# Optimization experiments

Measured on AMD Instinct MI355X. Metric: run time of the kernel, lower is better.

The kernel has to match this reference:

```python
import jax, jax.numpy as jnp
import numpy as np

N, F_IN, H1, H2, HEADS, E = 8192, 512, 128, 64, 3, 262144
NEG_SLOPE = 0.2  # PyG GATConv default negative_slope


def _add_self_loops(src, dst, n):
    loop = jnp.arange(n, dtype=src.dtype)
    return jnp.concatenate([src, loop]), jnp.concatenate([dst, loop])


def _gcn_conv(x, src, dst, W, b, n):
    # PyG GCNConv: h = x @ W, add self-loops, symmetric D^-1/2 A D^-1/2 aggregation, + bias
    h = x @ W
    s, d = _add_self_loops(src, dst, n)
    deg = jax.ops.segment_sum(jnp.ones(s.shape, h.dtype), d, num_segments=n)
    dinv = jnp.where(deg > 0, jax.lax.rsqrt(deg), 0.0)
    norm = dinv[s] * dinv[d]  # [E']
    return jax.ops.segment_sum(h[s] * norm[:, None], d, num_segments=n) + b


def _gat_conv(x, src, dst, W, a_src, a_dst, b, n, heads, concat):
    # PyG GATConv: per-head linear, LeakyReLU attention logits, segment softmax over
    # incoming edges per destination node, weighted scatter-aggregate.
    out_dim = W.shape[1] // heads
    h = (x @ W).reshape(n, heads, out_dim)  # [N, H, D]
    s, d = _add_self_loops(src, dst, n)
    a_s = jnp.einsum('nhd,hd->nh', h, a_src)
    a_d = jnp.einsum('nhd,hd->nh', h, a_dst)
    e = jax.nn.leaky_relu(a_s[s] + a_d[d], NEG_SLOPE)  # [E', H]
    m = jax.ops.segment_max(e, d, num_segments=n)      # stable softmax per dst segment
    ex = jnp.exp(e - m[d])
    den = jax.ops.segment_sum(ex, d, num_segments=n)
    msg = h[s] * (ex / den[d])[..., None]              # [E', H, D]
    out = jax.ops.segment_sum(msg, d, num_segments=n)  # [N, H, D]
    if concat:
        return out.reshape(n, heads * out_dim) + b
    return out.mean(axis=1) + b


def _forward(x, edge_index, gcn_W1, gcn_b1, gcn_Wmu, gcn_bmu, gcn_Wlv, gcn_blv,
             gat_W1, gat_as1, gat_ad1, gat_b1,
             gat_Wmu, gat_asmu, gat_admu, gat_bmu,
             gat_Wlv, gat_aslv, gat_adlv, gat_blv,
             eps_gcn, eps_gat):
    src, dst = edge_index[0], edge_index[1]
    n = x.shape[0]
    mu_g = lv_g = z_g = None
    for i in range(gcn_W1.shape[0]):  # gcn branches
        h = jax.nn.relu(_gcn_conv(x, src, dst, gcn_W1[i], gcn_b1[i], n))
        mu = _gcn_conv(h, src, dst, gcn_Wmu[i], gcn_bmu[i], n)
        lv = _gcn_conv(h, src, dst, gcn_Wlv[i], gcn_blv[i], n)
        z = mu + eps_gcn[i] * jnp.exp(lv)  # faithful: logvar passed as logstd
        mu_g = mu if mu_g is None else jnp.maximum(mu_g, mu)
        lv_g = lv if lv_g is None else jnp.maximum(lv_g, lv)
        z_g = z if z_g is None else jnp.maximum(z_g, z)
    mu_a = lv_a = z_a = None
    for i in range(gat_W1.shape[0]):  # gat branches
        h = jax.nn.relu(_gat_conv(x, src, dst, gat_W1[i], gat_as1[i], gat_ad1[i], gat_b1[i], n, HEADS, True))
        mu = _gat_conv(h, src, dst, gat_Wmu[i], gat_asmu[i], gat_admu[i], gat_bmu[i], n, HEADS, False)
        lv = _gat_conv(h, src, dst, gat_Wlv[i], gat_aslv[i], gat_adlv[i], gat_blv[i], n, HEADS, False)
        z = mu + eps_gat[i] * jnp.exp(lv)
        mu_a = mu if mu_a is None else jnp.maximum(mu_a, mu)
        lv_a = lv if lv_a is None else jnp.maximum(lv_a, lv)
        z_a = z if z_a is None else jnp.maximum(z_a, z)
    mu_max = jnp.maximum(mu_g, mu_a)
    lv_max = jnp.maximum(lv_g, lv_a)
    z_max = jnp.maximum(z_g, z_a)
    adj = jax.nn.sigmoid(z_max @ z_max.T)  # InnerProductDecoder.forward_all(sigmoid=True)
    return adj, mu_max, lv_max


def setup_inputs():
    key = jax.random.key(0)
    ki = iter(jax.random.split(key, 32))
    p = lambda shape: jax.random.normal(next(ki), shape, dtype=jnp.float32) * 0.05
    x = jax.random.normal(next(ki), (N, F_IN), dtype=jnp.float32)
    edge_index = jax.random.randint(next(ki), (2, E), 0, N)
    return dict(
        x=x, edge_index=edge_index,
        gcn_W1=p((2, F_IN, H1)), gcn_b1=p((2, H1)),
        gcn_Wmu=p((2, H1, H2)), gcn_bmu=p((2, H2)),
        gcn_Wlv=p((2, H1, H2)), gcn_blv=p((2, H2)),
        gat_W1=p((2, F_IN, HEADS * H1)), gat_as1=p((2, HEADS, H1)),
        gat_ad1=p((2, HEADS, H1)), gat_b1=p((2, HEADS * H1)),
        gat_Wmu=p((2, HEADS * H1, HEADS * H2)), gat_asmu=p((2, HEADS, H2)),
        gat_admu=p((2, HEADS, H2)), gat_bmu=p((2, H2)),
        gat_Wlv=p((2, HEADS * H1, HEADS * H2)), gat_aslv=p((2, HEADS, H2)),
        gat_adlv=p((2, HEADS, H2)), gat_blv=p((2, H2)),
        eps_gcn=jax.random.normal(next(ki), (2, N, H2), dtype=jnp.float32),
        eps_gat=jax.random.normal(next(ki), (2, N, H2), dtype=jnp.float32),
    )


def reference(x, edge_index, gcn_W1, gcn_b1, gcn_Wmu, gcn_bmu, gcn_Wlv, gcn_blv,
              gat_W1, gat_as1, gat_ad1, gat_b1,
              gat_Wmu, gat_asmu, gat_admu, gat_bmu,
              gat_Wlv, gat_aslv, gat_adlv, gat_blv,
              eps_gcn, eps_gat):
    return _forward(x, edge_index, gcn_W1, gcn_b1, gcn_Wmu, gcn_bmu, gcn_Wlv, gcn_blv,
                    gat_W1, gat_as1, gat_ad1, gat_b1,
                    gat_Wmu, gat_asmu, gat_admu, gat_bmu,
                    gat_Wlv, gat_aslv, gat_adlv, gat_blv,
                    eps_gcn, eps_gat)
```

## Files before the change

kernel.cpp:

```cpp
#include <hip/hip_runtime.h>
#include <hip/hip_bf16.h>
#include <math.h>
#include <stddef.h>

#define NN 8192
#define NEG_SLOPE 0.2f

typedef _Float16 h8 __attribute__((ext_vector_type(8)));
typedef __attribute__((ext_vector_type(4))) float f32x4;

__device__ __forceinline__ float lrelu(float x) { return x > 0.f ? x : NEG_SLOPE * x; }
__device__ __forceinline__ float sigf(float x) { return 1.f / (1.f + __expf(-x)); }

__device__ __forceinline__ unsigned short f16b(float x) {
    _Float16 h = (_Float16)x;
    unsigned short u;
    __builtin_memcpy(&u, &h, 2);
    return u;
}
__device__ __forceinline__ float f16f(unsigned short u) {
    _Float16 h;
    __builtin_memcpy(&h, &u, 2);
    return (float)h;
}
__device__ __forceinline__ void splith(float x, unsigned short& hu, unsigned short& lu) {
    _Float16 h = (_Float16)x;
    float hf = (float)h;
    _Float16 l = (_Float16)(x - hf);
    __builtin_memcpy(&hu, &h, 2);
    __builtin_memcpy(&lu, &l, 2);
}
__device__ __forceinline__ float2 unpkh(unsigned int v) {
    float2 r;
    r.x = f16f((unsigned short)(v & 0xffffu));
    r.y = f16f((unsigned short)(v >> 16));
    return r;
}
__device__ __forceinline__ unsigned int packh(float a, float b) {
    return (unsigned int)f16b(a) | ((unsigned int)f16b(b) << 16);
}

__device__ __forceinline__ void gll16(const unsigned short* g, unsigned short* l) {
    __builtin_amdgcn_global_load_lds(
        (const __attribute__((address_space(1))) unsigned int*)g,
        (__attribute__((address_space(3))) unsigned int*)l, 16, 0, 0);
}

__global__ void k_zero(int* __restrict__ p, int n) {
    int i = blockIdx.x * blockDim.x + threadIdx.x;
    if (i < n) p[i] = 0;
}
__global__ void k_count(const int* __restrict__ dst, int* __restrict__ cnt, int E) {
    int i = blockIdx.x * blockDim.x + threadIdx.x;
    if (i < E) atomicAdd(&cnt[dst[i]], 1);
}
__global__ void k_dinv(const int* __restrict__ cnt, float* __restrict__ dinv) {
    int i = blockIdx.x * blockDim.x + threadIdx.x;
    if (i < NN) dinv[i] = rsqrtf((float)(cnt[i] + 1));
}
__global__ void k_scan(const int* __restrict__ cnt, int* __restrict__ row_ptr) {
    __shared__ int part[1024];
    int t = threadIdx.x;
    int base = t * 8;
    int loc[8];
    int s = 0;
    #pragma unroll
    for (int j = 0; j < 8; ++j) { loc[j] = s; s += cnt[base + j]; }
    part[t] = s;
    __syncthreads();
    for (int off = 1; off < 1024; off <<= 1) {
        int v = (t >= off) ? part[t - off] : 0;
        __syncthreads();
        part[t] += v;
        __syncthreads();
    }
    int pre = (t == 0) ? 0 : part[t - 1];
    #pragma unroll
    for (int j = 0; j < 8; ++j) row_ptr[base + j] = pre + loc[j];
    if (t == 1023) row_ptr[NN] = part[1023];
}
__global__ void k_fill(const int* __restrict__ src, const int* __restrict__ dst,
                       const int* __restrict__ row_ptr, int* __restrict__ cursor,
                       int* __restrict__ csr_src, int E) {
    int i = blockIdx.x * blockDim.x + threadIdx.x;
    if (i < E) {
        int d = dst[i];
        csr_src[row_ptr[d] + atomicAdd(&cursor[d], 1)] = src[i];
    }
}

__global__ void k_cvt_x(const float* __restrict__ x, unsigned short* __restrict__ xh) {
    int i = blockIdx.x * 256 + threadIdx.x;
    int m = i >> 7, k4 = (i & 127) * 4;
    float4 v = *(const float4*)(x + (size_t)m * 512 + k4);
    ushort4 o;
    o.x = f16b(v.x); o.y = f16b(v.y); o.z = f16b(v.z); o.w = f16b(v.w);
    *(ushort4*)&xh[(size_t)m * 512 + k4] = o;
}

__global__ void k_wT(const float* __restrict__ W, unsigned short* __restrict__ Wt,
                     int K, int N, size_t wt_z_stride, int noff, int noff_z) {
    int b = blockIdx.z;
    W += (size_t)b * K * N;
    Wt += (size_t)b * wt_z_stride;
    int rowbase = noff + b * noff_z;
    int k0 = blockIdx.x * 32, n0 = blockIdx.y * 32;
    __shared__ float tl[32][33];
    int tid = threadIdx.x;
    int r = tid >> 5, cc = tid & 31;
    #pragma unroll
    for (int c = 0; c < 4; ++c)
        tl[r + c * 8][cc] = W[(size_t)(k0 + r + c * 8) * N + n0 + cc];
    __syncthreads();
    #pragma unroll
    for (int c = 0; c < 4; ++c) {
        int n = r + c * 8, k = cc;
        Wt[(size_t)(rowbase + n0 + n) * K + k0 + k] = f16b(tl[k][n]);
    }
}

template <int ROWS>
__device__ __forceinline__ void stage(const unsigned short* __restrict__ gbase, int lda,
                                      unsigned short* lds, int wid, int lane) {
    #pragma unroll
    for (int c = 0; c < ROWS / 32; ++c) {
        int chunk = c * 4 + wid;
        int row = chunk * 8 + (lane >> 3);
        int g = (lane & 7) ^ (row & 7);
        gll16(gbase + (size_t)row * lda + g * 8, lds + chunk * 512);
    }
}
__device__ __forceinline__ h8 fragrh(const unsigned short* lds, int row, int kg) {
    return *(const h8*)(lds + row * 64 + ((kg ^ (row & 7)) * 8));
}

template <int TERMS, int EPI>
__global__ __launch_bounds__(256) void k_gemm2(
    const unsigned short* __restrict__ A2, size_t azs, int lda,
    const unsigned short* __restrict__ B2, size_t bzs, int ldb,
    void* __restrict__ Cv, size_t czs, int ldc, int K) {
    __shared__ __align__(16) unsigned short sAh[128 * 64];
    __shared__ __align__(16) unsigned short sBh[64 * 64];
    __shared__ __align__(16) unsigned short sAl[(TERMS == 3) ? 128 * 64 : 8];
    __shared__ __align__(16) unsigned short sBl[(TERMS == 3) ? 64 * 64 : 8];
    const int tid = threadIdx.x;
    const int wid = tid >> 6, lane = tid & 63;
    const int wr = wid >> 1, wc = wid & 1;
    const int lr = lane & 15, lg = lane >> 4;
    const int m0 = blockIdx.x * 128, n0 = blockIdx.y * 64;
    const int z = blockIdx.z;
    A2 += (size_t)z * azs;
    B2 += (size_t)z * bzs;

    const f32x4 zero4 = {0.f, 0.f, 0.f, 0.f};
    f32x4 acc[4][2];
    #pragma unroll
    for (int m = 0; m < 4; ++m)
        #pragma unroll
        for (int n = 0; n < 2; ++n) acc[m][n] = zero4;

    for (int k0 = 0; k0 < K; k0 += 64) {
        stage<128>(A2 + (size_t)m0 * lda + k0, lda, sAh, wid, lane);
        stage<64> (B2 + (size_t)n0 * ldb + k0, ldb, sBh, wid, lane);
        if (TERMS == 3) {
            stage<128>(A2 + (size_t)m0 * lda + K + k0, lda, sAl, wid, lane);
            stage<64> (B2 + (size_t)n0 * ldb + K + k0, ldb, sBl, wid, lane);
        }
        __syncthreads();
        #pragma unroll
        for (int ks = 0; ks < 2; ++ks) {
            const int kg = ks * 4 + lg;
            h8 ah[4], al[4], bh[2], bl[2];
            #pragma unroll
            for (int m = 0; m < 4; ++m) {
                int row = wr * 64 + m * 16 + lr;
                ah[m] = fragrh(sAh, row, kg);
                if (TERMS == 3) al[m] = fragrh(sAl, row, kg);
            }
            #pragma unroll
            for (int n = 0; n < 2; ++n) {
                int row = wc * 32 + n * 16 + lr;
                bh[n] = fragrh(sBh, row, kg);
                if (TERMS == 3) bl[n] = fragrh(sBl, row, kg);
            }
            #pragma unroll
            for (int m = 0; m < 4; ++m)
                #pragma unroll
                for (int n = 0; n < 2; ++n) {
                    acc[m][n] = __builtin_amdgcn_mfma_f32_16x16x32_f16(ah[m], bh[n], acc[m][n], 0, 0, 0);
                    if (TERMS == 3) {
                        acc[m][n] = __builtin_amdgcn_mfma_f32_16x16x32_f16(al[m], bh[n], acc[m][n], 0, 0, 0);
                        acc[m][n] = __builtin_amdgcn_mfma_f32_16x16x32_f16(ah[m], bl[n], acc[m][n], 0, 0, 0);
                    }
                }
        }
        __syncthreads();
    }
    #pragma unroll
    for (int m = 0; m < 4; ++m)
        #pragma unroll
        for (int n = 0; n < 2; ++n)
            #pragma unroll
            for (int j = 0; j < 4; ++j) {
                int row = m0 + wr * 64 + m * 16 + lg * 4 + j;
                int col = n0 + wc * 32 + n * 16 + lr;
                float o = acc[m][n][j];
                if (EPI == 1) {
                    ((float*)Cv + (size_t)z * czs)[(size_t)row * ldc + col] = sigf(o);
                } else if (EPI == 2) {
                    ((unsigned short*)Cv + (size_t)z * czs)[(size_t)row * ldc + col] = f16b(o);
                } else {
                    ((float*)Cv + (size_t)z * czs)[(size_t)row * ldc + col] = o;
                }
            }
}

__global__ void k_gcn_a1(const uint2* __restrict__ xw2, const float* __restrict__ dinv,
                         const int* __restrict__ rp, const int* __restrict__ cs,
                         const float* __restrict__ b1, uint2* __restrict__ hb2) {
    int d = blockIdx.x;
    int t = threadIdx.x;
    float dd = dinv[d];
    uint2 sv = xw2[(size_t)d * 64 + t];
    float2 s0 = unpkh(sv.x), s1 = unpkh(sv.y);
    float a0 = dd * s0.x, a1 = dd * s0.y, a2 = dd * s1.x, a3 = dd * s1.y;
    int e0 = rp[d], e1 = rp[d + 1];
    int j = e0;
    for (; j + 4 <= e1; j += 4) {
        int i0 = cs[j], i1 = cs[j + 1], i2 = cs[j + 2], i3 = cs[j + 3];
        float w0 = dinv[i0], w1 = dinv[i1], w2 = dinv[i2], w3 = dinv[i3];
        uint2 v0 = xw2[(size_t)i0 * 64 + t];
        uint2 v1 = xw2[(size_t)i1 * 64 + t];
        uint2 v2 = xw2[(size_t)i2 * 64 + t];
        uint2 v3 = xw2[(size_t)i3 * 64 + t];
        float2 p;
        p = unpkh(v0.x); a0 += w0 * p.x; a1 += w0 * p.y;
        p = unpkh(v0.y); a2 += w0 * p.x; a3 += w0 * p.y;
        p = unpkh(v1.x); a0 += w1 * p.x; a1 += w1 * p.y;
        p = unpkh(v1.y); a2 += w1 * p.x; a3 += w1 * p.y;
        p = unpkh(v2.x); a0 += w2 * p.x; a1 += w2 * p.y;
        p = unpkh(v2.y); a2 += w2 * p.x; a3 += w2 * p.y;
        p = unpkh(v3.x); a0 += w3 * p.x; a1 += w3 * p.y;
        p = unpkh(v3.y); a2 += w3 * p.x; a3 += w3 * p.y;
    }
    for (; j < e1; ++j) {
        int s = cs[j];
        float w = dinv[s];
        uint2 v = xw2[(size_t)s * 64 + t];
        float2 p;
        p = unpkh(v.x); a0 += w * p.x; a1 += w * p.y;
        p = unpkh(v.y); a2 += w * p.x; a3 += w * p.y;
    }
    int c = 4 * t;
    float o0 = fmaxf(dd * a0 + b1[c], 0.f);
    float o1 = fmaxf(dd * a1 + b1[c + 1], 0.f);
    float o2 = fmaxf(dd * a2 + b1[c + 2], 0.f);
    float o3 = fmaxf(dd * a3 + b1[c + 3], 0.f);
    uint2 o;
    o.x = packh(o0, o1);
    o.y = packh(o2, o3);
    hb2[(size_t)d * 64 + t] = o;
}

__global__ void k_gcn_a2(const uint2* __restrict__ hb2, const float* __restrict__ dinv,
                         const int* __restrict__ rp, const int* __restrict__ cs,
                         uint2* __restrict__ hA2) {
    int d = blockIdx.x;
    int t = threadIdx.x;
    float dd = dinv[d];
    uint2 sv = hb2[(size_t)d * 64 + t];
    float2 s0 = unpkh(sv.x), s1 = unpkh(sv.y);
    float a0 = dd * s0.x, a1 = dd * s0.y, a2 = dd * s1.x, a3 = dd * s1.y;
    int e0 = rp[d], e1 = rp[d + 1];
    int j = e0;
    for (; j + 4 <= e1; j += 4) {
        int i0 = cs[j], i1 = cs[j + 1], i2 = cs[j + 2], i3 = cs[j + 3];
        float w0 = dinv[i0], w1 = dinv[i1], w2 = dinv[i2], w3 = dinv[i3];
        uint2 v0 = hb2[(size_t)i0 * 64 + t];
        uint2 v1 = hb2[(size_t)i1 * 64 + t];
        uint2 v2 = hb2[(size_t)i2 * 64 + t];
        uint2 v3 = hb2[(size_t)i3 * 64 + t];
        float2 p;
        p = unpkh(v0.x); a0 += w0 * p.x; a1 += w0 * p.y;
        p = unpkh(v0.y); a2 += w0 * p.x; a3 += w0 * p.y;
        p = unpkh(v1.x); a0 += w1 * p.x; a1 += w1 * p.y;
        p = unpkh(v1.y); a2 += w1 * p.x; a3 += w1 * p.y;
        p = unpkh(v2.x); a0 += w2 * p.x; a1 += w2 * p.y;
        p = unpkh(v2.y); a2 += w2 * p.x; a3 += w2 * p.y;
        p = unpkh(v3.x); a0 += w3 * p.x; a1 += w3 * p.y;
        p = unpkh(v3.y); a2 += w3 * p.x; a3 += w3 * p.y;
    }
    for (; j < e1; ++j) {
        int s = cs[j];
        float w = dinv[s];
        uint2 v = hb2[(size_t)s * 64 + t];
        float2 p;
        p = unpkh(v.x); a0 += w * p.x; a1 += w * p.y;
        p = unpkh(v.y); a2 += w * p.x; a3 += w * p.y;
    }
    uint2 o;
    o.x = packh(dd * a0, dd * a1);
    o.y = packh(dd * a2, dd * a3);
    hA2[(size_t)d * 64 + t] = o;
}

__global__ void k_gat_log1(const unsigned int* __restrict__ xwu, const float* __restrict__ a_s,
                           const float* __restrict__ a_d, float* __restrict__ as_n,
                           float* __restrict__ ad_n) {
    int br = blockIdx.z;
    int n = blockIdx.x;
    int hd = threadIdx.x >> 6, lane = threadIdx.x & 63;
    const unsigned int* hp = xwu + (size_t)n * 384 + br * 192 + hd * 64;
    const float* av = a_s + br * 384 + hd * 128;
    const float* dv = a_d + br * 384 + hd * 128;
    float2 f = unpkh(hp[lane]);
    float ss = f.x * av[2 * lane] + f.y * av[2 * lane + 1];
    float sd = f.x * dv[2 * lane] + f.y * dv[2 * lane + 1];
    #pragma unroll
    for (int off = 32; off; off >>= 1) {
        ss += __shfl_down(ss, off);
        sd += __shfl_down(sd, off);
    }
    if (lane == 0) {
        as_n[(size_t)br * NN * 3 + n * 3 + hd] = ss;
        ad_n[(size_t)br * NN * 3 + n * 3 + hd] = sd;
    }
}

__global__ void k_gat_log2(const unsigned short* __restrict__ h2gb, const float* __restrict__ asmu,
                           const float* __restrict__ aslv, const float* __restrict__ admu,
                           const float* __restrict__ adlv, float* __restrict__ as_n,
                           float* __restrict__ ad_n) {
    int zz = blockIdx.z;
    int br = zz >> 1, mt = zz & 1;
    int n = blockIdx.x;
    int hd = threadIdx.x >> 6, lane = threadIdx.x & 63;
    const unsigned short* hp = h2gb + (size_t)br * NN * 384 + (size_t)n * 384 + mt * 192 + hd * 64;
    const float* av = (mt ? aslv : asmu) + br * 192 + hd * 64;
    const float* dv = (mt ? adlv : admu) + br * 192 + hd * 64;
    float hv = f16f(hp[lane]);
    float ss = hv * av[lane];
    float sd = hv * dv[lane];
    #pragma unroll
    for (int off = 32; off; off >>= 1) {
        ss += __shfl_down(ss, off);
        sd += __shfl_down(sd, off);
    }
    if (lane == 0) {
        as_n[(size_t)zz * NN * 3 + n * 3 + hd] = ss;
        ad_n[(size_t)zz * NN * 3 + n * 3 + hd] = sd;
    }
}

__global__ void k_gat_attn(const float* __restrict__ as_n, const float* __restrict__ ad_n,
                           const int* __restrict__ rp, const int* __restrict__ cs,
                           float* __restrict__ w_csr, float* __restrict__ w_self, int E3) {
    int zz = blockIdx.z;
    as_n += (size_t)zz * NN * 3;
    ad_n += (size_t)zz * NN * 3;
    w_csr += (size_t)zz * E3;
    w_self += (size_t)zz * NN * 3;
    int d = blockIdx.x;
    int hd = threadIdx.x >> 6, lane = threadIdx.x & 63;
    int e0 = rp[d], e1 = rp[d + 1];
    float add = ad_n[d * 3 + hd];
    float eself = lrelu(as_n[d * 3 + hd] + add);
    float mx = eself;
    for (int j = e0 + lane; j < e1; j += 64) {
        float e = lrelu(as_n[cs[j] * 3 + hd] + add);
        w_csr[(size_t)j * 3 + hd] = e;
        mx = fmaxf(mx, e);
    }
    #pragma unroll
    for (int off = 32; off; off >>= 1) mx = fmaxf(mx, __shfl_xor(mx, off));
    float sm = (lane == 0) ? __expf(eself - mx) : 0.f;
    for (int j = e0 + lane; j < e1; j += 64)
        sm += __expf(w_csr[(size_t)j * 3 + hd] - mx);
    #pragma unroll
    for (int off = 32; off; off >>= 1) sm += __shfl_xor(sm, off);
    float inv = 1.f / sm;
    if (lane == 0) w_self[d * 3 + hd] = __expf(eself - mx) * inv;
    for (int j = e0 + lane; j < e1; j += 64)
        w_csr[(size_t)j * 3 + hd] = __expf(w_csr[(size_t)j * 3 + hd] - mx) * inv;
}

__global__ void k_gat_agg1(const uint2* __restrict__ xw2, const float* __restrict__ w_csr,
                           const float* __restrict__ w_self, const int* __restrict__ rp,
                           const int* __restrict__ cs, const float* __restrict__ b1,
                           uint2* __restrict__ h1s2, int E3) {
    int d = blockIdx.x;
    int t = threadIdx.x;
    int br = t >= 96 ? 1 : 0;
    int c = 4 * t - br * 384;
    int hd = c >> 7;
    const float* wc = w_csr + (size_t)br * E3;
    float ws = w_self[(size_t)br * NN * 3 + d * 3 + hd];
    uint2 sv = xw2[(size_t)d * 192 + t];
    float2 s0 = unpkh(sv.x), s1 = unpkh(sv.y);
    float a0 = ws * s0.x, a1 = ws * s0.y, a2 = ws * s1.x, a3 = ws * s1.y;
    int e0 = rp[d], e1 = rp[d + 1];
    int j = e0;
    for (; j + 4 <= e1; j += 4) {
        int i0 = cs[j], i1 = cs[j + 1], i2 = cs[j + 2], i3 = cs[j + 3];
        float w0 = wc[(size_t)(j + 0) * 3 + hd];
        float w1 = wc[(size_t)(j + 1) * 3 + hd];
        float w2 = wc[(size_t)(j + 2) * 3 + hd];
        float w3 = wc[(size_t)(j + 3) * 3 + hd];
        uint2 v0 = xw2[(size_t)i0 * 192 + t];
        uint2 v1 = xw2[(size_t)i1 * 192 + t];
        uint2 v2 = xw2[(size_t)i2 * 192 + t];
        uint2 v3 = xw2[(size_t)i3 * 192 + t];
        float2 p;
        p = unpkh(v0.x); a0 += w0 * p.x; a1 += w0 * p.y;
        p = unpkh(v0.y); a2 += w0 * p.x; a3 += w0 * p.y;
        p = unpkh(v1.x); a0 += w1 * p.x; a1 += w1 * p.y;
        p = unpkh(v1.y); a2 += w1 * p.x; a3 += w1 * p.y;
        p = unpkh(v2.x); a0 += w2 * p.x; a1 += w2 * p.y;
        p = unpkh(v2.y); a2 += w2 * p.x; a3 += w2 * p.y;
        p = unpkh(v3.x); a0 += w3 * p.x; a1 += w3 * p.y;
        p = unpkh(v3.y); a2 += w3 * p.x; a3 += w3 * p.y;
    }
    for (; j < e1; ++j) {
        int s = cs[j];
        float w = wc[(size_t)j * 3 + hd];
        uint2 v = xw2[(size_t)s * 192 + t];
        float2 p;
        p = unpkh(v.x); a0 += w * p.x; a1 += w * p.y;
        p = unpkh(v.y); a2 += w * p.x; a3 += w * p.y;
    }
    int cg = 4 * t;
    float o0 = fmaxf(a0 + b1[cg], 0.f);
    float o1 = fmaxf(a1 + b1[cg + 1], 0.f);
    float o2 = fmaxf(a2 + b1[cg + 2], 0.f);
    float o3 = fmaxf(a3 + b1[cg + 3], 0.f);
    uint2 o;
    o.x = packh(o0, o1);
    o.y = packh(o2, o3);
    h1s2[(size_t)d * 192 + t] = o;
}

__global__ void k_gat_agg2(const uint2* __restrict__ h2g2, const float* __restrict__ w_csr,
                           const float* __restrict__ w_self, const int* __restrict__ rp,
                           const int* __restrict__ cs, const float* __restrict__ bmu,
                           const float* __restrict__ blv, float* __restrict__ mt_gat, int E3) {
    int d = blockIdx.x;
    int t = threadIdx.x;
    int br = t >= 96 ? 1 : 0;
    int tb = t - br * 96;
    int mt = tb >= 48 ? 1 : 0;
    int c = 4 * tb - mt * 192;
    int hd = c >> 6;
    const float* wc = w_csr + (size_t)(br * 2 + mt) * E3;
    float ws = w_self[(size_t)(br * 2 + mt) * NN * 3 + d * 3 + hd];
    const uint2* hp = h2g2 + (size_t)br * NN * 96;
    uint2 sv = hp[(size_t)d * 96 + tb];
    float2 s0 = unpkh(sv.x), s1 = unpkh(sv.y);
    float a0 = ws * s0.x, a1 = ws * s0.y, a2 = ws * s1.x, a3 = ws * s1.y;
    int e0 = rp[d], e1 = rp[d + 1];
    int j = e0;
    for (; j + 4 <= e1; j += 4) {
        int i0 = cs[j], i1 = cs[j + 1], i2 = cs[j + 2], i3 = cs[j + 3];
        float w0 = wc[(size_t)(j + 0) * 3 + hd];
        float w1 = wc[(size_t)(j + 1) * 3 + hd];
        float w2 = wc[(size_t)(j + 2) * 3 + hd];
        float w3 = wc[(size_t)(j + 3) * 3 + hd];
        uint2 v0 = hp[(size_t)i0 * 96 + tb];
        uint2 v1 = hp[(size_t)i1 * 96 + tb];
        uint2 v2 = hp[(size_t)i2 * 96 + tb];
        uint2 v3 = hp[(size_t)i3 * 96 + tb];
        float2 p;
        p = unpkh(v0.x); a0 += w0 * p.x; a1 += w0 * p.y;
        p = unpkh(v0.y); a2 += w0 * p.x; a3 += w0 * p.y;
        p = unpkh(v1.x); a0 += w1 * p.x; a1 += w1 * p.y;
        p = unpkh(v1.y); a2 += w1 * p.x; a3 += w1 * p.y;
        p = unpkh(v2.x); a0 += w2 * p.x; a1 += w2 * p.y;
        p = unpkh(v2.y); a2 += w2 * p.x; a3 += w2 * p.y;
        p = unpkh(v3.x); a0 += w3 * p.x; a1 += w3 * p.y;
        p = unpkh(v3.y); a2 += w3 * p.x; a3 += w3 * p.y;
    }
    for (; j < e1; ++j) {
        int s = cs[j];
        float w = wc[(size_t)j * 3 + hd];
        uint2 v = hp[(size_t)s * 96 + tb];
        float2 p;
        p = unpkh(v.x); a0 += w * p.x; a1 += w * p.y;
        p = unpkh(v.y); a2 += w * p.x; a3 += w * p.y;
    }
    __shared__ float red[768];
    int rb = br * 384 + mt * 192 + c;
    red[rb] = a0; red[rb + 1] = a1; red[rb + 2] = a2; red[rb + 3] = a3;
    __syncthreads();
    if (t < 128) {
        #pragma unroll
        for (int q = 0; q < 2; ++q) {
            int o = t + q * 128;
            int obr = o >> 7, omt = (o >> 6) & 1, dd = o & 63;
            int base = obr * 384 + omt * 192;
            float tot = red[base + dd] + red[base + 64 + dd] + red[base + 128 + dd];
            const float* bias = omt ? blv : bmu;
            float v = tot * (1.f / 3.f) + bias[obr * 64 + dd];
            mt_gat[((size_t)(obr * 2 + omt) * NN + d) * 64 + dd] = v;
        }
    }
}

__global__ void k_finalize(const float* __restrict__ muv_gcn, const float* __restrict__ gcn_bmu,
                           const float* __restrict__ gcn_blv, const float* __restrict__ mt_gat,
                           const float* __restrict__ eps_gcn, const float* __restrict__ eps_gat,
                           float* __restrict__ mu_o, float* __restrict__ lv_o,
                           unsigned short* __restrict__ z2) {
    int i = blockIdx.x * 256 + threadIdx.x;
    int d = i >> 6, c = i & 63;
    const size_t NN64 = (size_t)NN * 64;
    float mu, lv, zm;
    {
        float m = muv_gcn[(size_t)d * 128 + c] + gcn_bmu[c];
        float l = muv_gcn[(size_t)d * 128 + 64 + c] + gcn_blv[c];
        float z = m + eps_gcn[i] * __expf(l);
        mu = m; lv = l; zm = z;
    }
    {
        float m = muv_gcn[NN64 * 2 + (size_t)d * 128 + c] + gcn_bmu[64 + c];
        float l = muv_gcn[NN64 * 2 + (size_t)d * 128 + 64 + c] + gcn_blv[64 + c];
        float z = m + eps_gcn[NN64 + i] * __expf(l);
        mu = fmaxf(mu, m); lv = fmaxf(lv, l); zm = fmaxf(zm, z);
    }
    #pragma unroll
    for (int br = 0; br < 2; ++br) {
        float m = mt_gat[(size_t)(br * 2 + 0) * NN64 + i];
        float l = mt_gat[(size_t)(br * 2 + 1) * NN64 + i];
        float z = m + eps_gat[(size_t)br * NN64 + i] * __expf(l);
        mu = fmaxf(mu, m); lv = fmaxf(lv, l); zm = fmaxf(zm, z);
    }
    mu_o[i] = mu;
    lv_o[i] = lv;
    unsigned short hh, ll;
    splith(zm, hh, ll);
    z2[(size_t)d * 128 + c] = hh;
    z2[(size_t)d * 128 + 64 + c] = ll;
}

extern "C" void kernel_launch(void* const* d_in, const int* in_sizes, int n_in,
                              void* d_out, int out_size, void* d_ws, size_t ws_size,
                              hipStream_t stream) {
    const float* x  = (const float*)d_in[0];
    const int*   ei = (const int*)d_in[1];
    const int E = in_sizes[1] / 2;
    const int E3 = E * 3;
    const int* src = ei;
    const int* dst = ei + E;

    const float* gcn_W1  = (const float*)d_in[2];
    const float* gcn_b1  = (const float*)d_in[3];
    const float* gcn_Wmu = (const float*)d_in[4];
    const float* gcn_bmu = (const float*)d_in[5];
    const float* gcn_Wlv = (const float*)d_in[6];
    const float* gcn_blv = (const float*)d_in[7];
    const float* gat_W1  = (const float*)d_in[8];
    const float* gat_as1 = (const float*)d_in[9];
    const float* gat_ad1 = (const float*)d_in[10];
    const float* gat_b1  = (const float*)d_in[11];
    const float* gat_Wmu = (const float*)d_in[12];
    const float* gat_asmu= (const float*)d_in[13];
    const float* gat_admu= (const float*)d_in[14];
    const float* gat_bmu = (const float*)d_in[15];
    const float* gat_Wlv = (const float*)d_in[16];
    const float* gat_aslv= (const float*)d_in[17];
    const float* gat_adlv= (const float*)d_in[18];
    const float* gat_blv = (const float*)d_in[19];
    const float* eps_gcn = (const float*)d_in[20];
    const float* eps_gat = (const float*)d_in[21];

    char* p = (char*)d_ws;
    auto alloc = [&](size_t bytes) {
        void* r = (void*)p;
        p += (bytes + 255) & ~(size_t)255;
        return r;
    };
    int*   cnt     = (int*)alloc((size_t)NN * 4);
    int*   cursor  = (int*)alloc((size_t)NN * 4);
    int*   row_ptr = (int*)alloc((size_t)(NN + 1) * 4);
    int*   csr_src = (int*)alloc((size_t)E * 4);
    float* dinv    = (float*)alloc((size_t)NN * 4);
    float* as_n1   = (float*)alloc((size_t)2 * NN * 3 * 4);
    float* ad_n1   = (float*)alloc((size_t)2 * NN * 3 * 4);
    float* wself1  = (float*)alloc((size_t)2 * NN * 3 * 4);
    float* wcsr1   = (float*)alloc((size_t)2 * E3 * 4);
    float* as_n2   = (float*)alloc((size_t)4 * NN * 3 * 4);
    float* ad_n2   = (float*)alloc((size_t)4 * NN * 3 * 4);
    float* wself2  = (float*)alloc((size_t)4 * NN * 3 * 4);
    float* wcsr2   = (float*)alloc((size_t)4 * E3 * 4);
    unsigned short* x2h      = (unsigned short*)alloc((size_t)NN * 512 * 2);
    unsigned short* wt_gcn1  = (unsigned short*)alloc((size_t)256 * 512 * 2);
    unsigned short* wt_gcnmuv= (unsigned short*)alloc((size_t)2 * 128 * 128 * 2);
    unsigned short* wt_gat1  = (unsigned short*)alloc((size_t)768 * 512 * 2);
    unsigned short* wt_gatmuv= (unsigned short*)alloc((size_t)2 * 384 * 384 * 2);
    unsigned short* xwb  = (unsigned short*)alloc((size_t)NN * 768 * 2);
    unsigned short* hb   = (unsigned short*)alloc((size_t)NN * 256 * 2);
    unsigned short* hA   = (unsigned short*)alloc((size_t)NN * 256 * 2);
    float* muv_gcn = (float*)alloc((size_t)2 * NN * 128 * 4);
    unsigned short* h1s  = (unsigned short*)alloc((size_t)NN * 768 * 2);
    unsigned short* h2gb = (unsigned short*)alloc((size_t)2 * NN * 384 * 2);
    float* mt_gat  = (float*)alloc((size_t)4 * NN * 64 * 4);
    unsigned short* z2 = (unsigned short*)alloc((size_t)NN * 128 * 2);

    float* adj  = (float*)d_out;
    float* mu_o = adj + (size_t)NN * NN;
    float* lv_o = mu_o + (size_t)NN * 64;

    k_zero<<<(2 * NN + 255) / 256, 256, 0, stream>>>(cnt, 2 * NN);
    k_count<<<(E + 255) / 256, 256, 0, stream>>>(dst, cnt, E);
    k_dinv<<<(NN + 255) / 256, 256, 0, stream>>>(cnt, dinv);
    k_scan<<<1, 1024, 0, stream>>>(cnt, row_ptr);
    k_fill<<<(E + 255) / 256, 256, 0, stream>>>(src, dst, row_ptr, cursor, csr_src, E);

    k_cvt_x<<<NN * 512 / 4 / 256, 256, 0, stream>>>(x, x2h);
    k_wT<<<dim3(16, 4, 2), 256, 0, stream>>>(gcn_W1, wt_gcn1, 512, 128, 0, 0, 128);
    k_wT<<<dim3(4, 2, 2), 256, 0, stream>>>(gcn_Wmu, wt_gcnmuv, 128, 64, (size_t)128 * 128, 0, 0);
    k_wT<<<dim3(4, 2, 2), 256, 0, stream>>>(gcn_Wlv, wt_gcnmuv, 128, 64, (size_t)128 * 128, 64, 0);
    k_wT<<<dim3(16, 12, 2), 256, 0, stream>>>(gat_W1, wt_gat1, 512, 384, 0, 0, 384);
    k_wT<<<dim3(12, 6, 2), 256, 0, stream>>>(gat_Wmu, wt_gatmuv, 384, 192, (size_t)384 * 384, 0, 0);
    k_wT<<<dim3(12, 6, 2), 256, 0, stream>>>(gat_Wlv, wt_gatmuv, 384, 192, (size_t)384 * 384, 192, 0);

    k_gemm2<1, 2><<<dim3(64, 4, 1), 256, 0, stream>>>(x2h, 0, 512, wt_gcn1, 0, 512,
                                                      xwb, 0, 256, 512);
    k_gcn_a1<<<NN, 64, 0, stream>>>((const uint2*)xwb, dinv, row_ptr, csr_src, gcn_b1,
                                    (uint2*)hb);
    k_gcn_a2<<<NN, 64, 0, stream>>>((const uint2*)hb, dinv, row_ptr, csr_src, (uint2*)hA);
    k_gemm2<1, 0><<<dim3(64, 2, 2), 256, 0, stream>>>(hA, 128, 256, wt_gcnmuv,
                                                      (size_t)128 * 128, 128,
                                                      muv_gcn, (size_t)NN * 128, 128, 128);

    k_gemm2<1, 2><<<dim3(64, 12, 1), 256, 0, stream>>>(x2h, 0, 512, wt_gat1, 0, 512,
                                                       xwb, 0, 768, 512);
    k_gat_log1<<<dim3(NN, 1, 2), 192, 0, stream>>>((const unsigned int*)xwb, gat_as1,
                                                   gat_ad1, as_n1, ad_n1);
    k_gat_attn<<<dim3(NN, 1, 2), 192, 0, stream>>>(as_n1, ad_n1, row_ptr, csr_src,
                                                   wcsr1, wself1, E3);
    k_gat_agg1<<<NN, 192, 0, stream>>>((const uint2*)xwb, wcsr1, wself1, row_ptr, csr_src,
                                       gat_b1, (uint2*)h1s, E3);
    k_gemm2<1, 2><<<dim3(64, 6, 2), 256, 0, stream>>>(h1s, 384, 768, wt_gatmuv,
                                                      (size_t)384 * 384, 384,
                                                      h2gb, (size_t)NN * 384, 384, 384);
    k_gat_log2<<<dim3(NN, 1, 4), 192, 0, stream>>>(h2gb, gat_asmu, gat_aslv, gat_admu,
                                                   gat_adlv, as_n2, ad_n2);
    k_gat_attn<<<dim3(NN, 1, 4), 192, 0, stream>>>(as_n2, ad_n2, row_ptr, csr_src,
                                                   wcsr2, wself2, E3);
    k_gat_agg2<<<NN, 192, 0, stream>>>((const uint2*)h2gb, wcsr2, wself2, row_ptr, csr_src,
                                       gat_bmu, gat_blv, mt_gat, E3);

    k_finalize<<<NN * 64 / 256, 256, 0, stream>>>(muv_gcn, gcn_bmu, gcn_blv, mt_gat,
                                                  eps_gcn, eps_gat, mu_o, lv_o, z2);
    k_gemm2<3, 1><<<dim3(64, 128, 1), 256, 0, stream>>>(z2, 0, 128, z2, 0, 128,
                                                        adj, 0, NN, 64);
}
```

Baseline: 364.8 us.

## Fuse GAT softmax into aggregation, drop one split-fp16 term, nontemporal adj stores

Merges the GAT attention-softmax kernel with the aggregation kernel for both layers. Edge indices and normalized weights are kept in shared memory, capped per node with a recompute fallback for high degree, so the per-edge weight arrays no longer go through global memory and two launches are removed. The final z·zᵀ GEMM drops from three split-fp16 MFMA terms to two (hi·hi + lo·hi), which cuts MFMA work and B-side lo staging but loses some precision. The sigmoid adjacency output is written with nontemporal stores to reduce cache pollution.

```diff
diff --git a/kernel.cpp b/kernel.cpp
--- a/kernel.cpp
+++ b/kernel.cpp
@@ -5,6 +5,7 @@
 
 #define NN 8192
 #define NEG_SLOPE 0.2f
+#define CAP 256
 
 typedef _Float16 h8 __attribute__((ext_vector_type(8)));
 typedef __attribute__((ext_vector_type(4))) float f32x4;
@@ -141,8 +142,8 @@
     void* __restrict__ Cv, size_t czs, int ldc, int K) {
     __shared__ __align__(16) unsigned short sAh[128 * 64];
     __shared__ __align__(16) unsigned short sBh[64 * 64];
-    __shared__ __align__(16) unsigned short sAl[(TERMS == 3) ? 128 * 64 : 8];
-    __shared__ __align__(16) unsigned short sBl[(TERMS == 3) ? 64 * 64 : 8];
+    __shared__ __align__(16) unsigned short sAl[(TERMS >= 2) ? 128 * 64 : 8];
+    __shared__ __align__(16) unsigned short sBl[(TERMS >= 3) ? 64 * 64 : 8];
     const int tid = threadIdx.x;
     const int wid = tid >> 6, lane = tid & 63;
     const int wr = wid >> 1, wc = wid & 1;
@@ -162,10 +163,8 @@
     for (int k0 = 0; k0 < K; k0 += 64) {
         stage<128>(A2 + (size_t)m0 * lda + k0, lda, sAh, wid, lane);
         stage<64> (B2 + (size_t)n0 * ldb + k0, ldb, sBh, wid, lane);
-        if (TERMS == 3) {
-            stage<128>(A2 + (size_t)m0 * lda + K + k0, lda, sAl, wid, lane);
-            stage<64> (B2 + (size_t)n0 * ldb + K + k0, ldb, sBl, wid, lane);
-        }
+        if (TERMS >= 2) stage<128>(A2 + (size_t)m0 * lda + K + k0, lda, sAl, wid, lane);
+        if (TERMS >= 3) stage<64> (B2 + (size_t)n0 * ldb + K + k0, ldb, sBl, wid, lane);
         __syncthreads();
         #pragma unroll
         for (int ks = 0; ks < 2; ++ks) {
@@ -175,23 +174,23 @@
             for (int m = 0; m < 4; ++m) {
                 int row = wr * 64 + m * 16 + lr;
                 ah[m] = fragrh(sAh, row, kg);
-                if (TERMS == 3) al[m] = fragrh(sAl, row, kg);
+                if (TERMS >= 2) al[m] = fragrh(sAl, row, kg);
             }
             #pragma unroll
             for (int n = 0; n < 2; ++n) {
                 int row = wc * 32 + n * 16 + lr;
                 bh[n] = fragrh(sBh, row, kg);
-                if (TERMS == 3) bl[n] = fragrh(sBl, row, kg);
+                if (TERMS >= 3) bl[n] = fragrh(sBl, row, kg);
             }
             #pragma unroll
             for (int m = 0; m < 4; ++m)
                 #pragma unroll
                 for (int n = 0; n < 2; ++n) {
                     acc[m][n] = __builtin_amdgcn_mfma_f32_16x16x32_f16(ah[m], bh[n], acc[m][n], 0, 0, 0);
-                    if (TERMS == 3) {
+                    if (TERMS >= 2)
                         acc[m][n] = __builtin_amdgcn_mfma_f32_16x16x32_f16(al[m], bh[n], acc[m][n], 0, 0, 0);
+                    if (TERMS >= 3)
                         acc[m][n] = __builtin_amdgcn_mfma_f32_16x16x32_f16(ah[m], bl[n], acc[m][n], 0, 0, 0);
-                    }
                 }
         }
         __syncthreads();
@@ -206,7 +205,8 @@
                 int col = n0 + wc * 32 + n * 16 + lr;
                 float o = acc[m][n][j];
                 if (EPI == 1) {
-                    ((float*)Cv + (size_t)z * czs)[(size_t)row * ldc + col] = sigf(o);
+                    float* cp = (float*)Cv + (size_t)z * czs + (size_t)row * ldc + col;
+                    __builtin_nontemporal_store(sigf(o), cp);
                 } else if (EPI == 2) {
                     ((unsigned short*)Cv + (size_t)z * czs)[(size_t)row * ldc + col] = f16b(o);
                 } else {
@@ -352,155 +352,191 @@
     }
 }
 
-__global__ void k_gat_attn(const float* __restrict__ as_n, const float* __restrict__ ad_n,
-                           const int* __restrict__ rp, const int* __restrict__ cs,
-                           float* __restrict__ w_csr, float* __restrict__ w_self, int E3) {
-    int zz = blockIdx.z;
-    as_n += (size_t)zz * NN * 3;
-    ad_n += (size_t)zz * NN * 3;
-    w_csr += (size_t)zz * E3;
-    w_self += (size_t)zz * NN * 3;
-    int d = blockIdx.x;
-    int hd = threadIdx.x >> 6, lane = threadIdx.x & 63;
-    int e0 = rp[d], e1 = rp[d + 1];
-    float add = ad_n[d * 3 + hd];
-    float eself = lrelu(as_n[d * 3 + hd] + add);
-    float mx = eself;
-    for (int j = e0 + lane; j < e1; j += 64) {
-        float e = lrelu(as_n[cs[j] * 3 + hd] + add);
-        w_csr[(size_t)j * 3 + hd] = e;
-        mx = fmaxf(mx, e);
-    }
-    #pragma unroll
-    for (int off = 32; off; off >>= 1) mx = fmaxf(mx, __shfl_xor(mx, off));
-    float sm = (lane == 0) ? __expf(eself - mx) : 0.f;
-    for (int j = e0 + lane; j < e1; j += 64)
-        sm += __expf(w_csr[(size_t)j * 3 + hd] - mx);
-    #pragma unroll
-    for (int off = 32; off; off >>= 1) sm += __shfl_xor(sm, off);
-    float inv = 1.f / sm;
-    if (lane == 0) w_self[d * 3 + hd] = __expf(eself - mx) * inv;
-    for (int j = e0 + lane; j < e1; j += 64)
-        w_csr[(size_t)j * 3 + hd] = __expf(w_csr[(size_t)j * 3 + hd] - mx) * inv;
-}
-
-__global__ void k_gat_agg1(const uint2* __restrict__ xw2, const float* __restrict__ w_csr,
-                           const float* __restrict__ w_self, const int* __restrict__ rp,
-                           const int* __restrict__ cs, const float* __restrict__ b1,
-                           uint2* __restrict__ h1s2, int E3) {
+__global__ __launch_bounds__(384) void k_gat_fused1(
+    const unsigned int* __restrict__ xwu,
+    const float* __restrict__ as_n, const float* __restrict__ ad_n,
+    const int* __restrict__ rp, const int* __restrict__ cs,
+    const float* __restrict__ b1, unsigned int* __restrict__ h1su) {
     int d = blockIdx.x;
     int t = threadIdx.x;
-    int br = t >= 96 ? 1 : 0;
-    int c = 4 * t - br * 384;
-    int hd = c >> 7;
-    const float* wc = w_csr + (size_t)br * E3;
-    float ws = w_self[(size_t)br * NN * 3 + d * 3 + hd];
-    uint2 sv = xw2[(size_t)d * 192 + t];
-    float2 s0 = unpkh(sv.x), s1 = unpkh(sv.y);
-    float a0 = ws * s0.x, a1 = ws * s0.y, a2 = ws * s1.x, a3 = ws * s1.y;
+    int wv = t >> 6, lane = t & 63;
     int e0 = rp[d], e1 = rp[d + 1];
-    int j = e0;
-    for (; j + 4 <= e1; j += 4) {
-        int i0 = cs[j], i1 = cs[j + 1], i2 = cs[j + 2], i3 = cs[j + 3];
-        float w0 = wc[(size_t)(j + 0) * 3 + hd];
-        float w1 = wc[(size_t)(j + 1) * 3 + hd];
-        float w2 = wc[(size_t)(j + 2) * 3 + hd];
-        float w3 = wc[(size_t)(j + 3) * 3 + hd];
-        uint2 v0 = xw2[(size_t)i0 * 192 + t];
-        uint2 v1 = xw2[(size_t)i1 * 192 + t];
-        uint2 v2 = xw2[(size_t)i2 * 192 + t];
-        uint2 v3 = xw2[(size_t)i3 * 192 + t];
-        float2 p;
-        p = unpkh(v0.x); a0 += w0 * p.x; a1 += w0 * p.y;
-        p = unpkh(v0.y); a2 += w0 * p.x; a3 += w0 * p.y;
-        p = unpkh(v1.x); a0 += w1 * p.x; a1 += w1 * p.y;
-        p = unpkh(v1.y); a2 += w1 * p.x; a3 += w1 * p.y;
-        p = unpkh(v2.x); a0 += w2 * p.x; a1 += w2 * p.y;
-        p = unpkh(v2.y); a2 += w2 * p.x; a3 += w2 * p.y;
-        p = unpkh(v3.x); a0 += w3 * p.x; a1 += w3 * p.y;
-        p = unpkh(v3.y); a2 += w3 * p.x; a3 += w3 * p.y;
-    }
-    for (; j < e1; ++j) {
-        int s = cs[j];
-        float w = wc[(size_t)j * 3 + hd];
-        uint2 v = xw2[(size_t)s * 192 + t];
-        float2 p;
-        p = unpkh(v.x); a0 += w * p.x; a1 += w * p.y;
-        p = unpkh(v.y); a2 += w * p.x; a3 += w * p.y;
-    }
-    int cg = 4 * t;
-    float o0 = fmaxf(a0 + b1[cg], 0.f);
-    float o1 = fmaxf(a1 + b1[cg + 1], 0.f);
-    float o2 = fmaxf(a2 + b1[cg + 2], 0.f);
-    float o3 = fmaxf(a3 + b1[cg + 3], 0.f);
-    uint2 o;
-    o.x = packh(o0, o1);
-    o.y = packh(o2, o3);
-    h1s2[(size_t)d * 192 + t] = o;
-}
-
-__global__ void k_gat_agg2(const uint2* __restrict__ h2g2, const float* __restrict__ w_csr,
-                           const float* __restrict__ w_self, const int* __restrict__ rp,
-                           const int* __restrict__ cs, const float* __restrict__ bmu,
-                           const float* __restrict__ blv, float* __restrict__ mt_gat, int E3) {
+    int deg = e1 - e0;
+    int dcap = deg < CAP ? deg : CAP;
+    __shared__ int se[CAP];
+    __shared__ float ws[6][CAP];
+    __shared__ float wself[6], wmx[6], winv[6], wadd[6];
+    for (int q = t; q < dcap; q += 384) se[q] = cs[e0 + q];
+    __syncthreads();
+    {
+        int br = wv / 3, hd = wv - br * 3;
+        const float* asn = as_n + (size_t)br * NN * 3;
+        float add = ad_n[(size_t)br * NN * 3 + d * 3 + hd];
+        float eself = lrelu(asn[d * 3 + hd] + add);
+        float mx = eself;
+        for (int q = lane; q < deg; q += 64) {
+            int s = (q < dcap) ? se[q] : cs[e0 + q];
+            float e = lrelu(asn[s * 3 + hd] + add);
+            if (q < dcap) ws[wv][q] = e;
+            mx = fmaxf(mx, e);
+        }
+        #pragma unroll
+        for (int off = 32; off; off >>= 1) mx = fmaxf(mx, __shfl_xor(mx, off));
+        float sm = (lane == 0) ? __expf(eself - mx) : 0.f;
+        for (int q = lane; q < deg; q += 64) {
+            float e = (q < dcap) ? ws[wv][q]
+                                 : lrelu(asn[cs[e0 + q] * 3 + hd] + add);
+            sm += __expf(e - mx);
+        }
+        #pragma unroll
+        for (int off = 32; off; off >>= 1) sm += __shfl_xor(sm, off);
+        float inv = 1.f / sm;
+        for (int q = lane; q < dcap; q += 64)
+            ws[wv][q] = __expf(ws[wv][q] - mx) * inv;
+        if (lane == 0) {
+            wself[wv] = __expf(eself - mx) * inv;
+            wmx[wv] = mx; winv[wv] = inv; wadd[wv] = add;
+        }
+    }
+    __syncthreads();
+    int br2 = t >= 192 ? 1 : 0;
+    int cu = t - br2 * 192;
+    int hd2 = cu >> 6;
+    int sw = br2 * 3 + hd2;
+    float a0, a1;
+    {
+        float2 p = unpkh(xwu[(size_t)d * 384 + t]);
+        float wsf = wself[sw];
+        a0 = wsf * p.x; a1 = wsf * p.y;
+    }
+    int q = 0;
+    for (; q + 4 <= dcap; q += 4) {
+        int s0 = se[q], s1 = se[q + 1], s2 = se[q + 2], s3 = se[q + 3];
+        float w0 = ws[sw][q], w1 = ws[sw][q + 1], w2 = ws[sw][q + 2], w3 = ws[sw][q + 3];
+        float2 p0 = unpkh(xwu[(size_t)s0 * 384 + t]);
+        float2 p1 = unpkh(xwu[(size_t)s1 * 384 + t]);
+        float2 p2 = unpkh(xwu[(size_t)s2 * 384 + t]);
+        float2 p3 = unpkh(xwu[(size_t)s3 * 384 + t]);
+        a0 += w0 * p0.x + w1 * p1.x + w2 * p2.x + w3 * p3.x;
+        a1 += w0 * p0.y + w1 * p1.y + w2 * p2.y + w3 * p3.y;
+    }
+    for (; q < dcap; ++q) {
+        float w = ws[sw][q];
+        float2 p = unpkh(xwu[(size_t)se[q] * 384 + t]);
+        a0 += w * p.x; a1 += w * p.y;
+    }
+    for (; q < deg; ++q) {
+        int s = cs[e0 + q];
+        const float* asn = as_n + (size_t)br2 * NN * 3;
+        float w = __expf(lrelu(asn[s * 3 + hd2] + wadd[sw]) - wmx[sw]) * winv[sw];
+        float2 p = unpkh(xwu[(size_t)s * 384 + t]);
+        a0 += w * p.x; a1 += w * p.y;
+    }
+    float o0 = fmaxf(a0 + b1[2 * t], 0.f);
+    float o1 = fmaxf(a1 + b1[2 * t + 1], 0.f);
+    h1su[(size_t)d * 384 + t] = packh(o0, o1);
+}
+
+__global__ __launch_bounds__(384) void k_gat_fused2(
+    const unsigned int* __restrict__ h2gu,
+    const float* __restrict__ as_n, const float* __restrict__ ad_n,
+    const int* __restrict__ rp, const int* __restrict__ cs,
+    const float* __restrict__ bmu, const float* __restrict__ blv,
+    float* __restrict__ mt_gat) {
     int d = blockIdx.x;
     int t = threadIdx.x;
-    int br = t >= 96 ? 1 : 0;
-    int tb = t - br * 96;
-    int mt = tb >= 48 ? 1 : 0;
-    int c = 4 * tb - mt * 192;
-    int hd = c >> 6;
-    const float* wc = w_csr + (size_t)(br * 2 + mt) * E3;
-    float ws = w_self[(size_t)(br * 2 + mt) * NN * 3 + d * 3 + hd];
-    const uint2* hp = h2g2 + (size_t)br * NN * 96;
-    uint2 sv = hp[(size_t)d * 96 + tb];
-    float2 s0 = unpkh(sv.x), s1 = unpkh(sv.y);
-    float a0 = ws * s0.x, a1 = ws * s0.y, a2 = ws * s1.x, a3 = ws * s1.y;
+    int wv = t >> 6, lane = t & 63;
     int e0 = rp[d], e1 = rp[d + 1];
-    int j = e0;
-    for (; j + 4 <= e1; j += 4) {
-        int i0 = cs[j], i1 = cs[j + 1], i2 = cs[j + 2], i3 = cs[j + 3];
-        float w0 = wc[(size_t)(j + 0) * 3 + hd];
-        float w1 = wc[(size_t)(j + 1) * 3 + hd];
-        float w2 = wc[(size_t)(j + 2) * 3 + hd];
-        float w3 = wc[(size_t)(j + 3) * 3 + hd];
-        uint2 v0 = hp[(size_t)i0 * 96 + tb];
-        uint2 v1 = hp[(size_t)i1 * 96 + tb];
-        uint2 v2 = hp[(size_t)i2 * 96 + tb];
-        uint2 v3 = hp[(size_t)i3 * 96 + tb];
-        float2 p;
-        p = unpkh(v0.x); a0 += w0 * p.x; a1 += w0 * p.y;
-        p = unpkh(v0.y); a2 += w0 * p.x; a3 += w0 * p.y;
-        p = unpkh(v1.x); a0 += w1 * p.x; a1 += w1 * p.y;
-        p = unpkh(v1.y); a2 += w1 * p.x; a3 += w1 * p.y;
-        p = unpkh(v2.x); a0 += w2 * p.x; a1 += w2 * p.y;
-        p = unpkh(v2.y); a2 += w2 * p.x; a3 += w2 * p.y;
-        p = unpkh(v3.x); a0 += w3 * p.x; a1 += w3 * p.y;
-        p = unpkh(v3.y); a2 += w3 * p.x; a3 += w3 * p.y;
-    }
-    for (; j < e1; ++j) {
-        int s = cs[j];
-        float w = wc[(size_t)j * 3 + hd];
-        uint2 v = hp[(size_t)s * 96 + tb];
-        float2 p;
-        p = unpkh(v.x); a0 += w * p.x; a1 += w * p.y;
-        p = unpkh(v.y); a2 += w * p.x; a3 += w * p.y;
+    int deg = e1 - e0;
+    int dcap = deg < CAP ? deg : CAP;
+    __shared__ int se[CAP];
+    __shared__ float ws[12][CAP];
+    __shared__ float wself[12], wmx[12], winv[12], wadd[12];
+    for (int q = t; q < dcap; q += 384) se[q] = cs[e0 + q];
+    __syncthreads();
+    #pragma unroll
+    for (int r = 0; r < 2; ++r) {
+        int sid = wv * 2 + r;
+        int zz = sid / 3, hd = sid - zz * 3;
+        const float* asn = as_n + (size_t)zz * NN * 3;
+        float add = ad_n[(size_t)zz * NN * 3 + d * 3 + hd];
+        float eself = lrelu(asn[d * 3 + hd] + add);
+        float mx = eself;
+        for (int q = lane; q < deg; q += 64) {
+            int s = (q < dcap) ? se[q] : cs[e0 + q];
+            float e = lrelu(asn[s * 3 + hd] + add);
+            if (q < dcap) ws[sid][q] = e;
+            mx = fmaxf(mx, e);
+        }
+        #pragma unroll
+        for (int off = 32; off; off >>= 1) mx = fmaxf(mx, __shfl_xor(mx, off));
+        float sm = (lane == 0) ? __expf(eself - mx) : 0.f;
+        for (int q = lane; q < deg; q += 64) {
+            float e = (q < dcap) ? ws[sid][q]
+                                 : lrelu(asn[cs[e0 + q] * 3 + hd] + add);
+            sm += __expf(e - mx);
+        }
+        #pragma unroll
+        for (int off = 32; off; off >>= 1) sm += __shfl_xor(sm, off);
+        float inv = 1.f / sm;
+        for (int q = lane; q < dcap; q += 64)
+            ws[sid][q] = __expf(ws[sid][q] - mx) * inv;
+        if (lane == 0) {
+            wself[sid] = __expf(eself - mx) * inv;
+            wmx[sid] = mx; winv[sid] = inv; wadd[sid] = add;
+        }
+    }
+    __syncthreads();
+    int br = t >= 192 ? 1 : 0;
+    int cu = t - br * 192;
+    int fc = 2 * cu;
+    int mt = fc >= 192 ? 1 : 0;
+    int cm = fc - mt * 192;
+    int hd2 = cm >> 6;
+    int sid = (br * 2 + mt) * 3 + hd2;
+    const unsigned int* hp = h2gu + (size_t)br * NN * 192;
+    float a0, a1;
+    {
+        float2 p = unpkh(hp[(size_t)d * 192 + cu]);
+        float wsf = wself[sid];
+        a0 = wsf * p.x; a1 = wsf * p.y;
+    }
+    int q = 0;
+    for (; q + 4 <= dcap; q += 4) {
+        int s0 = se[q], s1 = se[q + 1], s2 = se[q + 2], s3 = se[q + 3];
+        float w0 = ws[sid][q], w1 = ws[sid][q + 1], w2 = ws[sid][q + 2], w3 = ws[sid][q + 3];
+        float2 p0 = unpkh(hp[(size_t)s0 * 192 + cu]);
+        float2 p1 = unpkh(hp[(size_t)s1 * 192 + cu]);
+        float2 p2 = unpkh(hp[(size_t)s2 * 192 + cu]);
+        float2 p3 = unpkh(hp[(size_t)s3 * 192 + cu]);
+        a0 += w0 * p0.x + w1 * p1.x + w2 * p2.x + w3 * p3.x;
+        a1 += w0 * p0.y + w1 * p1.y + w2 * p2.y + w3 * p3.y;
+    }
+    for (; q < dcap; ++q) {
+        float w = ws[sid][q];
+        float2 p = unpkh(hp[(size_t)se[q] * 192 + cu]);
+        a0 += w * p.x; a1 += w * p.y;
+    }
+    for (; q < deg; ++q) {
+        int s = cs[e0 + q];
+        int zz = br * 2 + mt;
+        const float* asn = as_n + (size_t)zz * NN * 3;
+        float w = __expf(lrelu(asn[s * 3 + hd2] + wadd[sid]) - wmx[sid]) * winv[sid];
+        float2 p = unpkh(hp[(size_t)s * 192 + cu]);
+        a0 += w * p.x; a1 += w * p.y;
     }
     __shared__ float red[768];
-    int rb = br * 384 + mt * 192 + c;
-    red[rb] = a0; red[rb + 1] = a1; red[rb + 2] = a2; red[rb + 3] = a3;
+    int rb = br * 384 + mt * 192 + cm;
+    red[rb] = a0;
+    red[rb + 1] = a1;
     __syncthreads();
-    if (t < 128) {
-        #pragma unroll
-        for (int q = 0; q < 2; ++q) {
-            int o = t + q * 128;
-            int obr = o >> 7, omt = (o >> 6) & 1, dd = o & 63;
-            int base = obr * 384 + omt * 192;
-            float tot = red[base + dd] + red[base + 64 + dd] + red[base + 128 + dd];
-            const float* bias = omt ? blv : bmu;
-            float v = tot * (1.f / 3.f) + bias[obr * 64 + dd];
-            mt_gat[((size_t)(obr * 2 + omt) * NN + d) * 64 + dd] = v;
-        }
+    if (t < 256) {
+        int obr = t >> 7, omt = (t >> 6) & 1, dd = t & 63;
+        int base = obr * 384 + omt * 192;
+        float tot = red[base + dd] + red[base + 64 + dd] + red[base + 128 + dd];
+        const float* bias = omt ? blv : bmu;
+        float o = tot * (1.f / 3.f) + bias[obr * 64 + dd];
+        mt_gat[((size_t)(obr * 2 + omt) * NN + d) * 64 + dd] = o;
     }
 }
 
@@ -546,7 +582,6 @@
     const float* x  = (const float*)d_in[0];
     const int*   ei = (const int*)d_in[1];
     const int E = in_sizes[1] / 2;
-    const int E3 = E * 3;
     const int* src = ei;
     const int* dst = ei + E;
 
@@ -584,12 +619,8 @@
     float* dinv    = (float*)alloc((size_t)NN * 4);
     float* as_n1   = (float*)alloc((size_t)2 * NN * 3 * 4);
     float* ad_n1   = (float*)alloc((size_t)2 * NN * 3 * 4);
-    float* wself1  = (float*)alloc((size_t)2 * NN * 3 * 4);
-    float* wcsr1   = (float*)alloc((size_t)2 * E3 * 4);
     float* as_n2   = (float*)alloc((size_t)4 * NN * 3 * 4);
     float* ad_n2   = (float*)alloc((size_t)4 * NN * 3 * 4);
-    float* wself2  = (float*)alloc((size_t)4 * NN * 3 * 4);
-    float* wcsr2   = (float*)alloc((size_t)4 * E3 * 4);
     unsigned short* x2h      = (unsigned short*)alloc((size_t)NN * 512 * 2);
     unsigned short* wt_gcn1  = (unsigned short*)alloc((size_t)256 * 512 * 2);
     unsigned short* wt_gcnmuv= (unsigned short*)alloc((size_t)2 * 128 * 128 * 2);
@@ -635,22 +666,18 @@
                                                        xwb, 0, 768, 512);
     k_gat_log1<<<dim3(NN, 1, 2), 192, 0, stream>>>((const unsigned int*)xwb, gat_as1,
                                                    gat_ad1, as_n1, ad_n1);
-    k_gat_attn<<<dim3(NN, 1, 2), 192, 0, stream>>>(as_n1, ad_n1, row_ptr, csr_src,
-                                                   wcsr1, wself1, E3);
-    k_gat_agg1<<<NN, 192, 0, stream>>>((const uint2*)xwb, wcsr1, wself1, row_ptr, csr_src,
-                                       gat_b1, (uint2*)h1s, E3);
+    k_gat_fused1<<<NN, 384, 0, stream>>>((const unsigned int*)xwb, as_n1, ad_n1,
+                                         row_ptr, csr_src, gat_b1, (unsigned int*)h1s);
     k_gemm2<1, 2><<<dim3(64, 6, 2), 256, 0, stream>>>(h1s, 384, 768, wt_gatmuv,
                                                       (size_t)384 * 384, 384,
                                                       h2gb, (size_t)NN * 384, 384, 384);
     k_gat_log2<<<dim3(NN, 1, 4), 192, 0, stream>>>(h2gb, gat_asmu, gat_aslv, gat_admu,
                                                    gat_adlv, as_n2, ad_n2);
-    k_gat_attn<<<dim3(NN, 1, 4), 192, 0, stream>>>(as_n2, ad_n2, row_ptr, csr_src,
-                                                   wcsr2, wself2, E3);
-    k_gat_agg2<<<NN, 192, 0, stream>>>((const uint2*)h2gb, wcsr2, wself2, row_ptr, csr_src,
-                                       gat_bmu, gat_blv, mt_gat, E3);
+    k_gat_fused2<<<NN, 384, 0, stream>>>((const unsigned int*)h2gb, as_n2, ad_n2,
+                                         row_ptr, csr_src, gat_bmu, gat_blv, mt_gat);
 
     k_finalize<<<NN * 64 / 256, 256, 0, stream>>>(muv_gcn, gcn_bmu, gcn_blv, mt_gat,
                                                   eps_gcn, eps_gat, mu_o, lv_o, z2);
-    k_gemm2<3, 1><<<dim3(64, 128, 1), 256, 0, stream>>>(z2, 0, 128, z2, 0, 128,
+    k_gemm2<2, 1><<<dim3(64, 128, 1), 256, 0, stream>>>(z2, 0, 128, z2, 0, 128,
                                                         adj, 0, NN, 64);
 }
```

Measured after the change: 381.1 us. 4.5% more time.
